# Performance work log

Hardware: AMD Instinct MI355X
Metric: run time of the kernel (lower is better)

Reference implementation:

```python
import jax, jax.numpy as jnp
import numpy as np

EPS = 1e-08


def _phi(x, W):
    # Performer-style positive random features for the softmax kernel.
    # x: [..., d], W: [d, m]
    d = x.shape[-1]
    m = W.shape[-1]
    proj = jnp.einsum('...d,dm->...m', x, W) * (d ** -0.25)
    sq = jnp.sum(x * x, axis=-1, keepdims=True) / (2.0 * jnp.sqrt(jnp.float32(d)))
    return jnp.exp(proj - sq) * (m ** -0.5)


def setup_inputs() -> dict:
    key = jax.random.key(0)
    k1, k2, k3 = jax.random.split(key, 3)
    B, L, D = 8, 2048, 512
    K = 4
    m = 256
    content_amp = jax.random.normal(k1, (B, L, D), dtype=jnp.float32)
    style_amp = jax.random.normal(k2, (B, K, L, D), dtype=jnp.float32)
    W = jax.random.normal(k3, (D, m), dtype=jnp.float32)
    return {"content_amp": content_amp, "style_amp": style_amp, "W": W}


def reference(content_amp, style_amp, W):
    B, K, L, D = style_amp.shape
    style_seq = style_amp.reshape(B, K * L, D)          # [B, KL, D]
    phi_q = _phi(content_amp, W)                         # [B, Lq, m]
    phi_k = _phi(style_seq, W)                           # [B, KL, m]
    S = jnp.einsum('bkm,bkd->bmd', phi_k, style_seq)     # [B, m, D]
    Z = jnp.sum(phi_k, axis=1)                           # [B, m]
    num = jnp.einsum('blm,bmd->bld', phi_q, S)           # [B, Lq, D]
    den = jnp.einsum('blm,bm->bl', phi_q, Z)[..., None] + EPS
    f_a = num / den
    amp_updated = content_amp + f_a
    return (amp_updated, f_a)
```

## Files before the change

kernel.cpp:

```cpp
#include <hip/hip_runtime.h>
#include <hip/hip_bf16.h>
#include <math.h>

typedef short  s16x8 __attribute__((ext_vector_type(8)));
typedef short  s16x4 __attribute__((ext_vector_type(4)));
typedef float  f32x4 __attribute__((ext_vector_type(4)));

#define DD 512
#define MM 256
#define BB 8
#define LL 2048
#define KLT 8192
#define NSPLIT 8

#define S1f     0.21022410381342864f
#define INV2SDf 0.02209708691207961f
#define S2f     0.0625f
#define EPSV    1e-8f

__device__ __forceinline__ ushort f2b(float f) {
    __hip_bfloat16 h = __float2bfloat16(f);
    return *reinterpret_cast<ushort*>(&h);
}
__device__ __forceinline__ float b2f(ushort u) {
    union { unsigned u32; float f; } x; x.u32 = ((unsigned)u) << 16; return x.f;
}

__device__ __forceinline__ void gl_lds16(const ushort* g, ushort* l) {
    __builtin_amdgcn_global_load_lds(
        (const __attribute__((address_space(1))) unsigned int*)(const void*)g,
        (__attribute__((address_space(3))) unsigned int*)(void*)l,
        16, 0, 0);
}

__global__ __launch_bounds__(256) void convert_rows(const float* __restrict__ X,
                                                    ushort* __restrict__ Xb,
                                                    float* __restrict__ Sq) {
    const int row  = blockIdx.x * 4 + (threadIdx.x >> 6);
    const int lane = threadIdx.x & 63;
    const float4* src = (const float4*)(X + (size_t)row * DD);
    float4 v0 = src[lane];
    float4 v1 = src[lane + 64];
    float s = v0.x * v0.x + v0.y * v0.y + v0.z * v0.z + v0.w * v0.w
            + v1.x * v1.x + v1.y * v1.y + v1.z * v1.z + v1.w * v1.w;
    s16x4* dst = (s16x4*)(Xb + (size_t)row * DD);
    s16x4 o0, o1;
    o0[0] = (short)f2b(v0.x); o0[1] = (short)f2b(v0.y);
    o0[2] = (short)f2b(v0.z); o0[3] = (short)f2b(v0.w);
    o1[0] = (short)f2b(v1.x); o1[1] = (short)f2b(v1.y);
    o1[2] = (short)f2b(v1.z); o1[3] = (short)f2b(v1.w);
    dst[lane]      = o0;
    dst[lane + 64] = o1;
#pragma unroll
    for (int off = 32; off; off >>= 1) s += __shfl_down(s, off);
    if (lane == 0) Sq[row] = s * INV2SDf;
}

__global__ __launch_bounds__(256) void conv_style(const float* __restrict__ X,
                                                  ushort* __restrict__ Xb,
                                                  ushort* __restrict__ XT,
                                                  float* __restrict__ Sq) {
    __shared__ ushort lds[64 * 72];
    const int t = threadIdx.x;
    const int klt = blockIdx.x, dt = blockIdx.y, b = blockIdx.z;
    const int r = t >> 2, c0 = (t & 3) * 16;
    const size_t rowg = (size_t)b * KLT + klt * 64 + r;
    const float4* src = (const float4*)(X + rowg * DD + dt * 64 + c0);
    float s = 0.f;
    s16x8 o0, o1;
#pragma unroll
    for (int i = 0; i < 2; ++i) {
        float4 v = src[2 * i], w = src[2 * i + 1];
        s += v.x * v.x + v.y * v.y + v.z * v.z + v.w * v.w
           + w.x * w.x + w.y * w.y + w.z * w.z + w.w * w.w;
        s16x8 o;
        o[0] = (short)f2b(v.x); o[1] = (short)f2b(v.y);
        o[2] = (short)f2b(v.z); o[3] = (short)f2b(v.w);
        o[4] = (short)f2b(w.x); o[5] = (short)f2b(w.y);
        o[6] = (short)f2b(w.z); o[7] = (short)f2b(w.w);
        if (i == 0) o0 = o; else o1 = o;
    }
    ushort* dstb = Xb + rowg * DD + dt * 64 + c0;
    *(s16x8*)(dstb)     = o0;
    *(s16x8*)(dstb + 8) = o1;
    *(s16x8*)(lds + r * 72 + c0)     = o0;
    *(s16x8*)(lds + r * 72 + c0 + 8) = o1;
    s += __shfl_xor(s, 1);
    s += __shfl_xor(s, 2);
    if ((t & 3) == 0) atomicAdd(&Sq[rowg], s * INV2SDf);
    __syncthreads();
    const int d = t >> 2, k0c = (t & 3) * 16;
    s16x8 t0, t1;
#pragma unroll
    for (int j = 0; j < 8; ++j) t0[j] = (short)lds[(k0c + j) * 72 + d];
#pragma unroll
    for (int j = 0; j < 8; ++j) t1[j] = (short)lds[(k0c + 8 + j) * 72 + d];
    ushort* dstT = XT + ((size_t)b * DD + dt * 64 + d) * KLT + klt * 64 + k0c;
    *(s16x8*)(dstT)     = t0;
    *(s16x8*)(dstT + 8) = t1;
}

__global__ __launch_bounds__(256) void prep_w(const float* __restrict__ W,
                                              ushort* __restrict__ Wt) {
    __shared__ ushort lds[64 * 78];
    const int t = threadIdx.x;
    const int dt = blockIdx.x;
    const int mt = blockIdx.y;
    {
        int r = t >> 2, c0 = (t & 3) * 16;
        const float4* src = (const float4*)(W + (size_t)(dt * 64 + r) * MM + mt * 64 + c0);
#pragma unroll
        for (int i = 0; i < 4; ++i) {
            float4 v = src[i];
            lds[r * 78 + c0 + 4 * i + 0] = f2b(v.x);
            lds[r * 78 + c0 + 4 * i + 1] = f2b(v.y);
            lds[r * 78 + c0 + 4 * i + 2] = f2b(v.z);
            lds[r * 78 + c0 + 4 * i + 3] = f2b(v.w);
        }
    }
    __syncthreads();
    {
        int m = t >> 2, d0 = (t & 3) * 16;
        ushort* dst = Wt + (size_t)(mt * 64 + m) * DD + dt * 64 + d0;
#pragma unroll
        for (int j = 0; j < 16; ++j) dst[j] = lds[(d0 + j) * 78 + m];
    }
}

__device__ __forceinline__ void gemm128(const ushort* __restrict__ A, int lda,
                                        const ushort* __restrict__ B, int ldb,
                                        int rowbase, int colbase, int k0, int k1,
                                        ushort* sA, ushort* sB, f32x4 acc[4][4]) {
    const int t = threadIdx.x;
    const int l = t & 63, w = t >> 6;
    const int wr = (w >> 1) * 64, wc = (w & 1) * 64;
    const int fr = l & 15, fg = l >> 4;
    const int lrow = l >> 2, lk = (l & 3) * 8;

    for (int kk = k0; kk < k1; kk += 32) {
        gl_lds16(A + (size_t)(rowbase + w * 16 + lrow) * lda + kk + lk,
                 sA + (w * 16) * 32);
        gl_lds16(A + (size_t)(rowbase + (w + 4) * 16 + lrow) * lda + kk + lk,
                 sA + ((w + 4) * 16) * 32);
        gl_lds16(B + (size_t)(colbase + w * 16 + lrow) * ldb + kk + lk,
                 sB + (w * 16) * 32);
        gl_lds16(B + (size_t)(colbase + (w + 4) * 16 + lrow) * ldb + kk + lk,
                 sB + ((w + 4) * 16) * 32);
        __syncthreads();
        s16x8 a[4], b[4];
#pragma unroll
        for (int mi = 0; mi < 4; ++mi)
            a[mi] = *(const s16x8*)(sA + (wr + mi * 16 + fr) * 32 + fg * 8);
#pragma unroll
        for (int ni = 0; ni < 4; ++ni)
            b[ni] = *(const s16x8*)(sB + (wc + ni * 16 + fr) * 32 + fg * 8);
#pragma unroll
        for (int mi = 0; mi < 4; ++mi)
#pragma unroll
            for (int ni = 0; ni < 4; ++ni)
                acc[mi][ni] = __builtin_amdgcn_mfma_f32_16x16x32_bf16(
                    a[mi], b[ni], acc[mi][ni], 0, 0, 0);
        __syncthreads();
    }
}

__global__ __launch_bounds__(256) void phikt_gemm(const ushort* __restrict__ Wt,
                                                  const ushort* __restrict__ Sb,
                                                  const float* __restrict__ sqk,
                                                  ushort* __restrict__ PhiKT) {
    __shared__ __align__(16) ushort smem[128 * 64];
    ushort* sA = smem;
    ushort* sB = smem + 128 * 32;
    f32x4 acc[4][4] = {};
    const int rowbase = blockIdx.y * 128;
    const int colbase = blockIdx.x * 128;
    gemm128(Wt, DD, Sb, DD, rowbase, colbase, 0, DD, sA, sB, acc);

    const int t = threadIdx.x, l = t & 63, w = t >> 6;
    const int wr = (w >> 1) * 64, wc = (w & 1) * 64, fr = l & 15, fg = l >> 4;
    const int b = colbase >> 13;
    const int kll_base = colbase & (KLT - 1);
    float sqv[4];
#pragma unroll
    for (int ni = 0; ni < 4; ++ni) sqv[ni] = sqk[colbase + wc + ni * 16 + fr];

    for (int c = 0; c < 2; ++c) {
        if ((wr >> 6) == c) {
#pragma unroll
            for (int mi = 0; mi < 4; ++mi)
#pragma unroll
                for (int ni = 0; ni < 4; ++ni)
#pragma unroll
                    for (int rr = 0; rr < 4; ++rr)
                        smem[(mi * 16 + fg * 4 + rr) * 128 + wc + ni * 16 + fr] =
                            f2b(__expf(acc[mi][ni][rr] * S1f - sqv[ni]) * S2f);
        }
        __syncthreads();
        {
            const int row = t >> 2, col0 = (t & 3) * 32;
            const int m = rowbase + c * 64 + row;
            ushort* dst = PhiKT + ((size_t)b << 21) + ((size_t)m << 13) + kll_base + col0;
#pragma unroll
            for (int j = 0; j < 4; ++j)
                *(s16x8*)(dst + 8 * j) = *(s16x8*)&smem[row * 128 + col0 + 8 * j];
        }
        __syncthreads();
    }
}

__global__ __launch_bounds__(256) void phiq_gemm(const ushort* __restrict__ Cb,
                                                 const ushort* __restrict__ Wt,
                                                 const float* __restrict__ sqq,
                                                 ushort* __restrict__ PhiQ) {
    __shared__ __align__(16) ushort smem[128 * 64];
    ushort* sA = smem;
    ushort* sB = smem + 128 * 32;
    f32x4 acc[4][4] = {};
    const int rowbase = blockIdx.x * 128;
    const int colbase = blockIdx.y * 128;
    gemm128(Cb, DD, Wt, DD, rowbase, colbase, 0, DD, sA, sB, acc);

    const int t = threadIdx.x, l = t & 63, w = t >> 6;
    const int wr = (w >> 1) * 64, wc = (w & 1) * 64, fr = l & 15, fg = l >> 4;
    float sqr[4][4];
#pragma unroll
    for (int mi = 0; mi < 4; ++mi)
#pragma unroll
        for (int rr = 0; rr < 4; ++rr)
            sqr[mi][rr] = sqq[rowbase + wr + mi * 16 + fg * 4 + rr];

    for (int c = 0; c < 2; ++c) {
        if ((wr >> 6) == c) {
#pragma unroll
            for (int mi = 0; mi < 4; ++mi)
#pragma unroll
                for (int ni = 0; ni < 4; ++ni)
#pragma unroll
                    for (int rr = 0; rr < 4; ++rr)
                        smem[(mi * 16 + fg * 4 + rr) * 128 + wc + ni * 16 + fr] =
                            f2b(__expf(acc[mi][ni][rr] * S1f - sqr[mi][rr]) * S2f);
        }
        __syncthreads();
        {
            const int row = t >> 2, col0 = (t & 3) * 32;
            const int lg = rowbase + c * 64 + row;
            ushort* dst = PhiQ + (size_t)lg * MM + colbase + col0;
#pragma unroll
            for (int j = 0; j < 4; ++j)
                *(s16x8*)(dst + 8 * j) = *(s16x8*)&smem[row * 128 + col0 + 8 * j];
        }
        __syncthreads();
    }
}

__global__ __launch_bounds__(256) void s_gemm(const ushort* __restrict__ PhiKT,
                                              const ushort* __restrict__ StyT,
                                              float* __restrict__ Spart) {
    __shared__ __align__(16) ushort smem[128 * 64];
    ushort* sA = smem;
    ushort* sB = smem + 128 * 32;
    f32x4 acc[4][4] = {};
    const int b = blockIdx.z >> 3, split = blockIdx.z & 7;
    const int rowbase = blockIdx.x * 128;
    const int colbase = blockIdx.y * 128;
    const ushort* A = PhiKT + ((size_t)b << 21);
    const ushort* B = StyT + (size_t)b * DD * KLT;
    gemm128(A, KLT, B, KLT, rowbase, colbase, split * 1024, split * 1024 + 1024,
            sA, sB, acc);

    const int t = threadIdx.x, l = t & 63, w = t >> 6;
    const int wr = (w >> 1) * 64, wc = (w & 1) * 64, fr = l & 15, fg = l >> 4;
    float* ldsf = (float*)smem;
    float* out = Spart + (size_t)(split * BB + b) * MM * DD;

    for (int c = 0; c < 4; ++c) {
        const bool part = (wr == 0) ? (c < 2) : (c >= 2);
        const int c2 = (wr == 0) ? c : c - 2;
        if (part) {
#pragma unroll
            for (int mi2 = 0; mi2 < 2; ++mi2) {
                const int mi = 2 * c2 + mi2;
#pragma unroll
                for (int ni = 0; ni < 4; ++ni)
#pragma unroll
                    for (int rr = 0; rr < 4; ++rr)
                        ldsf[(mi2 * 16 + fg * 4 + rr) * 128 + wc + ni * 16 + fr] =
                            acc[mi][ni][rr];
            }
        }
        __syncthreads();
        {
            const int row = t >> 3, col0 = (t & 7) * 16;
            const int m = rowbase + c * 32 + row;
            float* dst = out + (size_t)m * DD + colbase + col0;
#pragma unroll
            for (int j = 0; j < 4; ++j)
                *(float4*)(dst + 4 * j) = *(float4*)&ldsf[row * 128 + col0 + 4 * j];
        }
        __syncthreads();
    }
}

__global__ __launch_bounds__(256) void s_fin(const float* __restrict__ Sp,
                                             ushort* __restrict__ St) {
    __shared__ ushort lds[64 * 78];
    const int t = threadIdx.x;
    const int mt = blockIdx.x, dt = blockIdx.y, b = blockIdx.z;
    {
        const int r = t >> 2, c0 = (t & 3) * 16;
        float accv[16];
#pragma unroll
        for (int j = 0; j < 16; ++j) accv[j] = 0.f;
#pragma unroll
        for (int sp = 0; sp < NSPLIT; ++sp) {
            const float4* src = (const float4*)(Sp +
                ((size_t)(sp * BB + b) * MM + mt * 64 + r) * DD + dt * 64 + c0);
#pragma unroll
            for (int i = 0; i < 4; ++i) {
                float4 v = src[i];
                accv[4 * i + 0] += v.x; accv[4 * i + 1] += v.y;
                accv[4 * i + 2] += v.z; accv[4 * i + 3] += v.w;
            }
        }
#pragma unroll
        for (int j = 0; j < 16; ++j) lds[r * 78 + c0 + j] = f2b(accv[j]);
    }
    __syncthreads();
    {
        const int d = t >> 2, m0 = (t & 3) * 16;
        ushort* dst = St + ((size_t)b * DD + dt * 64 + d) * MM + mt * 64 + m0;
#pragma unroll
        for (int j = 0; j < 16; ++j) dst[j] = lds[(m0 + j) * 78 + d];
    }
}

__global__ __launch_bounds__(256) void z_kernel(const ushort* __restrict__ PhiKT,
                                                float* __restrict__ Z) {
    const int row = blockIdx.x * 4 + (threadIdx.x >> 6);
    const int lane = threadIdx.x & 63;
    const int b = row >> 8, m = row & 255;
    const ushort* p = PhiKT + ((size_t)b << 21) + ((size_t)m << 13);
    float s = 0.f;
#pragma unroll
    for (int i = 0; i < 16; ++i) {
        s16x8 v = *(const s16x8*)(p + (size_t)(i * 64 + lane) * 8);
#pragma unroll
        for (int j = 0; j < 8; ++j) s += b2f((ushort)v[j]);
    }
#pragma unroll
    for (int off = 32; off; off >>= 1) s += __shfl_down(s, off);
    if (lane == 0) Z[row] = s;
}

__global__ __launch_bounds__(256) void den_kernel(const ushort* __restrict__ PhiQ,
                                                  const float* __restrict__ Z,
                                                  float* __restrict__ Den) {
    const int row = blockIdx.x * 4 + (threadIdx.x >> 6);
    const int lane = threadIdx.x & 63;
    const int b = row >> 11;
    s16x4 q = *(const s16x4*)(PhiQ + (size_t)row * MM + lane * 4);
    float4 z = *(const float4*)(Z + (size_t)b * MM + lane * 4);
    float s = b2f((ushort)q[0]) * z.x + b2f((ushort)q[1]) * z.y +
              b2f((ushort)q[2]) * z.z + b2f((ushort)q[3]) * z.w;
#pragma unroll
    for (int off = 32; off; off >>= 1) s += __shfl_down(s, off);
    if (lane == 0) Den[row] = s;
}

__global__ __launch_bounds__(256) void out_gemm(const ushort* __restrict__ PhiQ,
                                                const ushort* __restrict__ St,
                                                const float* __restrict__ Den,
                                                const float* __restrict__ Content,
                                                float* __restrict__ Amp,
                                                float* __restrict__ Fa) {
    __shared__ __align__(16) ushort smem[128 * 64];
    ushort* sA = smem;
    ushort* sB = smem + 128 * 32;
    f32x4 acc[4][4] = {};
    const int b = blockIdx.z;
    const int rowbase = blockIdx.x * 128;
    const int colbase = blockIdx.y * 128;
    const ushort* A = PhiQ + (size_t)b * LL * MM;
    const ushort* B = St + (size_t)b * DD * MM;
    gemm128(A, MM, B, MM, rowbase, colbase, 0, MM, sA, sB, acc);

    const int t = threadIdx.x, l = t & 63, w = t >> 6;
    const int wr = (w >> 1) * 64, wc = (w & 1) * 64, fr = l & 15, fg = l >> 4;
    float* ldsf = (float*)smem;

    for (int c = 0; c < 4; ++c) {
        const bool part = (wr == 0) ? (c < 2) : (c >= 2);
        const int c2 = (wr == 0) ? c : c - 2;
        if (part) {
#pragma unroll
            for (int mi2 = 0; mi2 < 2; ++mi2) {
                const int mi = 2 * c2 + mi2;
#pragma unroll
                for (int ni = 0; ni < 4; ++ni)
#pragma unroll
                    for (int rr = 0; rr < 4; ++rr)
                        ldsf[(mi2 * 16 + fg * 4 + rr) * 128 + wc + ni * 16 + fr] =
                            acc[mi][ni][rr];
            }
        }
        __syncthreads();
        {
            const int row = t >> 3, col0 = (t & 7) * 16;
            const int lg = b * LL + rowbase + c * 32 + row;
            const float inv = 1.0f / (Den[lg] + EPSV);
            const size_t base = (size_t)lg * DD + colbase + col0;
#pragma unroll
            for (int j = 0; j < 4; ++j) {
                float4 v = *(float4*)&ldsf[row * 128 + col0 + 4 * j];
                float4 f4 = {v.x * inv, v.y * inv, v.z * inv, v.w * inv};
                float4 c4 = *(const float4*)&Content[base + 4 * j];
                *(float4*)&Fa[base + 4 * j] = f4;
                float4 a4 = {c4.x + f4.x, c4.y + f4.y, c4.z + f4.z, c4.w + f4.w};
                *(float4*)&Amp[base + 4 * j] = a4;
            }
        }
        __syncthreads();
    }
}

extern "C" void kernel_launch(void* const* d_in, const int* in_sizes, int n_in,
                              void* d_out, int out_size, void* d_ws, size_t ws_size,
                              hipStream_t stream) {
    const float* content = (const float*)d_in[0];
    const float* style   = (const float*)d_in[1];
    const float* Wm      = (const float*)d_in[2];
    float* amp = (float*)d_out;
    float* fa  = (float*)d_out + (size_t)BB * LL * DD;

    ushort* styleT = (ushort*)d_out;

    float* wsf   = (float*)d_ws;
    float* Spart = wsf;
    float* sq_k  = Spart + (size_t)NSPLIT * BB * MM * DD;
    float* sq_q  = sq_k + (size_t)BB * KLT;
    float* Zbuf  = sq_q + (size_t)BB * LL;
    float* den   = Zbuf + (size_t)BB * MM;
    ushort* wsu     = (ushort*)(den + (size_t)BB * LL);
    ushort* style_b = wsu;
    ushort* cont_b  = style_b + (size_t)BB * KLT * DD;
    ushort* Wt      = cont_b + (size_t)BB * LL * DD;
    ushort* phi_kT  = Wt + (size_t)MM * DD;
    ushort* phi_q   = phi_kT + (size_t)BB * MM * KLT;
    ushort* St      = phi_q + (size_t)BB * LL * MM;

    hipMemsetAsync(sq_k, 0, (size_t)BB * KLT * sizeof(float), stream);

    prep_w<<<dim3(8, 4), 256, 0, stream>>>(Wm, Wt);
    convert_rows<<<(BB * LL) / 4, 256, 0, stream>>>(content, cont_b, sq_q);
    conv_style<<<dim3(KLT / 64, DD / 64, BB), 256, 0, stream>>>(style, style_b, styleT, sq_k);

    phikt_gemm<<<dim3((BB * KLT) / 128, MM / 128), 256, 0, stream>>>(Wt, style_b, sq_k, phi_kT);
    phiq_gemm<<<dim3((BB * LL) / 128, MM / 128), 256, 0, stream>>>(cont_b, Wt, sq_q, phi_q);

    z_kernel<<<(BB * MM) / 4, 256, 0, stream>>>(phi_kT, Zbuf);
    s_gemm<<<dim3(MM / 128, DD / 128, BB * NSPLIT), 256, 0, stream>>>(phi_kT, styleT, Spart);
    s_fin<<<dim3(MM / 64, DD / 64, BB), 256, 0, stream>>>(Spart, St);

    den_kernel<<<(BB * LL) / 4, 256, 0, stream>>>(phi_q, Zbuf, den);
    out_gemm<<<dim3(LL / 128, DD / 128, BB), 256, 0, stream>>>(phi_q, St, den, content, amp, fa);
}
```

Before: 416.3 us.

## Fuse Z reduction into phi_k GEMM, widen style conversion, remap grids for XCD locality

```diff
diff --git a/kernel.cpp b/kernel.cpp
--- a/kernel.cpp
+++ b/kernel.cpp
@@ -56,21 +56,26 @@
     if (lane == 0) Sq[row] = s * INV2SDf;
 }
 
+#define CS_PITCH 514
 __global__ __launch_bounds__(256) void conv_style(const float* __restrict__ X,
                                                   ushort* __restrict__ Xb,
                                                   ushort* __restrict__ XT,
                                                   float* __restrict__ Sq) {
-    __shared__ ushort lds[64 * 72];
+    __shared__ ushort lds[64 * CS_PITCH];
     const int t = threadIdx.x;
-    const int klt = blockIdx.x, dt = blockIdx.y, b = blockIdx.z;
-    const int r = t >> 2, c0 = (t & 3) * 16;
+    const int klt = blockIdx.x;
+    const int b   = blockIdx.y;
+    const int r = t >> 2;
+    const int q = t & 3;
     const size_t rowg = (size_t)b * KLT + klt * 64 + r;
-    const float4* src = (const float4*)(X + rowg * DD + dt * 64 + c0);
+    const float* srcf = X + rowg * DD;
+    ushort* dstb = Xb + rowg * DD;
     float s = 0.f;
-    s16x8 o0, o1;
-#pragma unroll
-    for (int i = 0; i < 2; ++i) {
-        float4 v = src[2 * i], w = src[2 * i + 1];
+#pragma unroll
+    for (int i = 0; i < 16; ++i) {
+        const int col = q * 8 + 32 * i;
+        float4 v = *(const float4*)(srcf + col);
+        float4 w = *(const float4*)(srcf + col + 4);
         s += v.x * v.x + v.y * v.y + v.z * v.z + v.w * v.w
            + w.x * w.x + w.y * w.y + w.z * w.z + w.w * w.w;
         s16x8 o;
@@ -78,26 +83,26 @@
         o[2] = (short)f2b(v.z); o[3] = (short)f2b(v.w);
         o[4] = (short)f2b(w.x); o[5] = (short)f2b(w.y);
         o[6] = (short)f2b(w.z); o[7] = (short)f2b(w.w);
-        if (i == 0) o0 = o; else o1 = o;
-    }
-    ushort* dstb = Xb + rowg * DD + dt * 64 + c0;
-    *(s16x8*)(dstb)     = o0;
-    *(s16x8*)(dstb + 8) = o1;
-    *(s16x8*)(lds + r * 72 + c0)     = o0;
-    *(s16x8*)(lds + r * 72 + c0 + 8) = o1;
+        *(s16x8*)(dstb + col) = o;
+        *(s16x8*)(lds + r * CS_PITCH + col) = o;
+    }
     s += __shfl_xor(s, 1);
     s += __shfl_xor(s, 2);
-    if ((t & 3) == 0) atomicAdd(&Sq[rowg], s * INV2SDf);
+    if (q == 0) Sq[rowg] = s * INV2SDf;
     __syncthreads();
-    const int d = t >> 2, k0c = (t & 3) * 16;
-    s16x8 t0, t1;
-#pragma unroll
-    for (int j = 0; j < 8; ++j) t0[j] = (short)lds[(k0c + j) * 72 + d];
-#pragma unroll
-    for (int j = 0; j < 8; ++j) t1[j] = (short)lds[(k0c + 8 + j) * 72 + d];
-    ushort* dstT = XT + ((size_t)b * DD + dt * 64 + d) * KLT + klt * 64 + k0c;
-    *(s16x8*)(dstT)     = t0;
-    *(s16x8*)(dstT + 8) = t1;
+#pragma unroll
+    for (int dd2 = 0; dd2 < 2; ++dd2) {
+        const int d = t + dd2 * 256;
+        s16x8 o[8];
+#pragma unroll
+        for (int jc = 0; jc < 8; ++jc)
+#pragma unroll
+            for (int je = 0; je < 8; ++je)
+                o[jc][je] = (short)lds[(jc * 8 + je) * CS_PITCH + d];
+        ushort* dst = XT + ((size_t)b * DD + d) * KLT + klt * 64;
+#pragma unroll
+        for (int k = 0; k < 8; ++k) *(s16x8*)(dst + 8 * k) = o[k];
+    }
 }
 
 __global__ __launch_bounds__(256) void prep_w(const float* __restrict__ W,
@@ -167,13 +172,16 @@
 __global__ __launch_bounds__(256) void phikt_gemm(const ushort* __restrict__ Wt,
                                                   const ushort* __restrict__ Sb,
                                                   const float* __restrict__ sqk,
-                                                  ushort* __restrict__ PhiKT) {
+                                                  ushort* __restrict__ PhiKT,
+                                                  float* __restrict__ Z) {
     __shared__ __align__(16) ushort smem[128 * 64];
     ushort* sA = smem;
     ushort* sB = smem + 128 * 32;
     f32x4 acc[4][4] = {};
-    const int rowbase = blockIdx.y * 128;
-    const int colbase = blockIdx.x * 128;
+    const int z = blockIdx.x;
+    const int kl_tile = (z & 7) * 64 + ((z >> 3) >> 1);
+    const int rowbase = ((z >> 3) & 1) * 128;
+    const int colbase = kl_tile * 128;
     gemm128(Wt, DD, Sb, DD, rowbase, colbase, 0, DD, sA, sB, acc);
 
     const int t = threadIdx.x, l = t & 63, w = t >> 6;
@@ -200,9 +208,17 @@
             const int row = t >> 2, col0 = (t & 3) * 32;
             const int m = rowbase + c * 64 + row;
             ushort* dst = PhiKT + ((size_t)b << 21) + ((size_t)m << 13) + kll_base + col0;
-#pragma unroll
-            for (int j = 0; j < 4; ++j)
-                *(s16x8*)(dst + 8 * j) = *(s16x8*)&smem[row * 128 + col0 + 8 * j];
+            float zp = 0.f;
+#pragma unroll
+            for (int j = 0; j < 4; ++j) {
+                s16x8 v = *(s16x8*)&smem[row * 128 + col0 + 8 * j];
+                *(s16x8*)(dst + 8 * j) = v;
+#pragma unroll
+                for (int e = 0; e < 8; ++e) zp += b2f((ushort)v[e]);
+            }
+            zp += __shfl_xor(zp, 1);
+            zp += __shfl_xor(zp, 2);
+            if ((t & 3) == 0) atomicAdd(&Z[b * MM + m], zp);
         }
         __syncthreads();
     }
@@ -216,8 +232,10 @@
     ushort* sA = smem;
     ushort* sB = smem + 128 * 32;
     f32x4 acc[4][4] = {};
-    const int rowbase = blockIdx.x * 128;
-    const int colbase = blockIdx.y * 128;
+    const int z = blockIdx.x;
+    const int lt = (z & 7) * 16 + ((z >> 3) >> 1);
+    const int rowbase = lt * 128;
+    const int colbase = ((z >> 3) & 1) * 128;
     gemm128(Cb, DD, Wt, DD, rowbase, colbase, 0, DD, sA, sB, acc);
 
     const int t = threadIdx.x, l = t & 63, w = t >> 6;
@@ -260,9 +278,12 @@
     ushort* sA = smem;
     ushort* sB = smem + 128 * 32;
     f32x4 acc[4][4] = {};
-    const int b = blockIdx.z >> 3, split = blockIdx.z & 7;
-    const int rowbase = blockIdx.x * 128;
-    const int colbase = blockIdx.y * 128;
+    const int z = blockIdx.x;
+    const int xcd = z & 7, slot = z >> 3;
+    const int g = xcd * 8 + (slot >> 3);
+    const int b = g >> 3, split = g & 7;
+    const int rowbase = ((slot >> 2) & 1) * 128;
+    const int colbase = (slot & 3) * 128;
     const ushort* A = PhiKT + ((size_t)b << 21);
     const ushort* B = StyT + (size_t)b * DD * KLT;
     gemm128(A, KLT, B, KLT, rowbase, colbase, split * 1024, split * 1024 + 1024,
@@ -332,24 +353,6 @@
 #pragma unroll
         for (int j = 0; j < 16; ++j) dst[j] = lds[(m0 + j) * 78 + d];
     }
-}
-
-__global__ __launch_bounds__(256) void z_kernel(const ushort* __restrict__ PhiKT,
-                                                float* __restrict__ Z) {
-    const int row = blockIdx.x * 4 + (threadIdx.x >> 6);
-    const int lane = threadIdx.x & 63;
-    const int b = row >> 8, m = row & 255;
-    const ushort* p = PhiKT + ((size_t)b << 21) + ((size_t)m << 13);
-    float s = 0.f;
-#pragma unroll
-    for (int i = 0; i < 16; ++i) {
-        s16x8 v = *(const s16x8*)(p + (size_t)(i * 64 + lane) * 8);
-#pragma unroll
-        for (int j = 0; j < 8; ++j) s += b2f((ushort)v[j]);
-    }
-#pragma unroll
-    for (int off = 32; off; off >>= 1) s += __shfl_down(s, off);
-    if (lane == 0) Z[row] = s;
 }
 
 __global__ __launch_bounds__(256) void den_kernel(const ushort* __restrict__ PhiQ,
@@ -377,9 +380,13 @@
     ushort* sA = smem;
     ushort* sB = smem + 128 * 32;
     f32x4 acc[4][4] = {};
-    const int b = blockIdx.z;
-    const int rowbase = blockIdx.x * 128;
-    const int colbase = blockIdx.y * 128;
+    const int z = blockIdx.x;
+    const int xcd = z & 7, slot = z >> 3;
+    const int g = xcd * 8 + (slot >> 3);
+    const int b = g >> 3, lpair = g & 7;
+    const int lt = lpair * 2 + ((slot >> 2) & 1);
+    const int rowbase = lt * 128;
+    const int colbase = (slot & 3) * 128;
     const ushort* A = PhiQ + (size_t)b * LL * MM;
     const ushort* B = St + (size_t)b * DD * MM;
     gemm128(A, MM, B, MM, rowbase, colbase, 0, MM, sA, sB, acc);
@@ -448,19 +455,18 @@
     ushort* phi_q   = phi_kT + (size_t)BB * MM * KLT;
     ushort* St      = phi_q + (size_t)BB * LL * MM;
 
-    hipMemsetAsync(sq_k, 0, (size_t)BB * KLT * sizeof(float), stream);
+    hipMemsetAsync(Zbuf, 0, (size_t)BB * MM * sizeof(float), stream);
 
     prep_w<<<dim3(8, 4), 256, 0, stream>>>(Wm, Wt);
     convert_rows<<<(BB * LL) / 4, 256, 0, stream>>>(content, cont_b, sq_q);
-    conv_style<<<dim3(KLT / 64, DD / 64, BB), 256, 0, stream>>>(style, style_b, styleT, sq_k);
-
-    phikt_gemm<<<dim3((BB * KLT) / 128, MM / 128), 256, 0, stream>>>(Wt, style_b, sq_k, phi_kT);
-    phiq_gemm<<<dim3((BB * LL) / 128, MM / 128), 256, 0, stream>>>(cont_b, Wt, sq_q, phi_q);
-
-    z_kernel<<<(BB * MM) / 4, 256, 0, stream>>>(phi_kT, Zbuf);
-    s_gemm<<<dim3(MM / 128, DD / 128, BB * NSPLIT), 256, 0, stream>>>(phi_kT, styleT, Spart);
+    conv_style<<<dim3(KLT / 64, BB), 256, 0, stream>>>(style, style_b, styleT, sq_k);
+
+    phikt_gemm<<<1024, 256, 0, stream>>>(Wt, style_b, sq_k, phi_kT, Zbuf);
+    phiq_gemm<<<256, 256, 0, stream>>>(cont_b, Wt, sq_q, phi_q);
+
+    s_gemm<<<512, 256, 0, stream>>>(phi_kT, styleT, Spart);
     s_fin<<<dim3(MM / 64, DD / 64, BB), 256, 0, stream>>>(Spart, St);
 
     den_kernel<<<(BB * LL) / 4, 256, 0, stream>>>(phi_q, Zbuf, den);
-    out_gemm<<<dim3(LL / 128, DD / 128, BB), 256, 0, stream>>>(phi_q, St, den, content, amp, fa);
-}
+    out_gemm<<<512, 256, 0, stream>>>(phi_q, St, den, content, amp, fa);
+}
```

New measurement: 409.5 us. Within noise of the previous version (-1.6%).
